# Kernel optimization log

Measured on AMD Instinct MI355X. Metric: run time of the kernel, lower is better.

## Reference

```python
import jax, jax.numpy as jnp
import numpy as np

N = 1024        # total atoms
H = 256         # hidden_dim
L = 512         # latent_dim
NG = 50         # n_gaussians
NI = 3          # n_interactions
CUTOFF = 5.0
MAXZ = 100
B = 16          # molecules (N // 64 atoms each)

CENTERS = jnp.linspace(0.0, CUTOFF, NG)
WIDTH = 0.5 * (CUTOFF / NG)   # scalar, same for all gaussians
LN_EPS = 1e-5

def gelu(x):
    return jax.nn.gelu(x, approximate=False)  # torch default GELU is exact erf

def setup_inputs() -> dict:
    key = jax.random.key(0)
    ks = jax.random.split(key, 24)
    s = 0.05
    inp = {
        'z': jax.random.randint(ks[0], (N,), 0, MAXZ),
        'pos': jax.random.uniform(ks[1], (N, 3), dtype=jnp.float32) * 10.0,  # 10 A box
        'batch': jnp.arange(N, dtype=jnp.int32) // (N // B),
        'emb': jax.random.normal(ks[2], (MAXZ, H), dtype=jnp.float32),
        # per-interaction params stacked over layer axis (NI)
        'fw1': jax.random.normal(ks[3], (NI, NG, H), dtype=jnp.float32) * s,
        'fb1': jnp.zeros((NI, H), jnp.float32),
        'fw2': jax.random.normal(ks[4], (NI, H, H), dtype=jnp.float32) * s,
        'fb2': jnp.zeros((NI, H), jnp.float32),
        'aw1': jax.random.normal(ks[5], (NI, H, H), dtype=jnp.float32) * s,
        'ab1': jnp.zeros((NI, H), jnp.float32),
        'aw2': jax.random.normal(ks[6], (NI, H, H), dtype=jnp.float32) * s,
        'ab2': jnp.zeros((NI, H), jnp.float32),
        # projection head
        'pw1': jax.random.normal(ks[7], (H, H), dtype=jnp.float32) * s,
        'pb1': jnp.zeros((H,), jnp.float32),
        'pw2': jax.random.normal(ks[8], (H, L), dtype=jnp.float32) * s,
        'pb2': jnp.zeros((L,), jnp.float32),
        'ln_g': jnp.ones((L,), jnp.float32),
        'ln_b': jnp.zeros((L,), jnp.float32),
    }
    return inp

def _interaction(h, pos, fw1, fb1, fw2, fb2, aw1, ab1, aw2, ab2):
    diff = pos[None, :, :] - pos[:, None, :]              # [N,N,3]
    dist = jnp.linalg.norm(diff, axis=-1)                  # [N,N]
    mask = (dist < CUTOFF) & (dist > 1e-6)                 # [N,N]
    rbf = jnp.exp(-((dist[..., None] - CENTERS) ** 2) / (2.0 * WIDTH ** 2))  # [N,N,NG]
    W = gelu(rbf @ fw1 + fb1) @ fw2 + fb2                  # [N,N,H] filter MLP
    Wm = W * mask[..., None].astype(W.dtype)
    # agg[i,c] = sum_j Wm[i,j,c] * h[j,c]
    agg = jnp.einsum('ijc,jc->ic', Wm, h)
    return gelu(agg @ aw1 + ab1) @ aw2 + ab2

def reference(z, pos, batch, emb, fw1, fb1, fw2, fb2, aw1, ab1, aw2, ab2,
              pw1, pb1, pw2, pb2, ln_g, ln_b):
    h = emb[z]                                             # [N,H]
    for i in range(NI):
        h = h + _interaction(h, pos, fw1[i], fb1[i], fw2[i], fb2[i],
                             aw1[i], ab1[i], aw2[i], ab2[i])
    pooled = jax.ops.segment_sum(h, batch, num_segments=B)  # [B,H]
    x = gelu(pooled @ pw1 + pb1) @ pw2 + pb2               # [B,L]
    mu = jnp.mean(x, axis=-1, keepdims=True)
    var = jnp.var(x, axis=-1, keepdims=True)
    return (x - mu) / jnp.sqrt(var + LN_EPS) * ln_g + ln_b
```

## Files before the change

### kernel.cpp

```cpp
#include <hip/hip_runtime.h>
#include <hip/hip_fp16.h>
#include <math.h>

#define N 1024
#define H 256
#define L 512
#define NG 50
#define NI 3
#define B 16
#define NBINS 2048
#define CUT 5.0f
#define BPB 16
#define TROWS (NBINS + 1)
#define MATB 4
#define CAP 768
#define APAD 264

typedef __attribute__((ext_vector_type(8))) short bf16x8;
typedef __attribute__((ext_vector_type(4))) float f32x4;

#define FMA4(A_, S_, V_) do { \
    (A_).x = fmaf((S_), (V_).x, (A_).x); (A_).y = fmaf((S_), (V_).y, (A_).y); \
    (A_).z = fmaf((S_), (V_).z, (A_).z); (A_).w = fmaf((S_), (V_).w, (A_).w); } while (0)

__device__ __forceinline__ float gelu_f(float x) {
    return 0.5f * x * (1.0f + erff(x * 0.70710678118654752f));
}
__device__ __forceinline__ unsigned short f2bf(float f) {
    unsigned u = __float_as_uint(f);
    unsigned r = (u + 0x7fffu + ((u >> 16) & 1u)) >> 16;
    return (unsigned short)r;
}

__global__ void __launch_bounds__(256) setup_k(
        const int* __restrict__ z, const float* __restrict__ emb,
        const float* __restrict__ pos, float* __restrict__ h,
        __half* __restrict__ hhf, int* __restrict__ meta,
        int* __restrict__ cnts, const float* __restrict__ fw2,
        unsigned short* __restrict__ Bt, __half* __restrict__ Wtb) {
    int tid = threadIdx.x;
    if (blockIdx.x >= N) {
        int blk = blockIdx.x - N;
        int l = blk / H, ch = blk % H;
        float v = fw2[((size_t)l * H + tid) * H + ch];
        Bt[((size_t)l * H + ch) * H + tid] = f2bf(v);
        if (tid == 0)
            Wtb[((size_t)l * TROWS + NBINS) * H + ch] = __float2half(0.f);
        return;
    }
    int i = blockIdx.x;
    float v = emb[z[i] * H + tid];
    h[i * H + tid] = v;
    hhf[i * H + tid] = __float2half(v);

    __shared__ int sCnt;
    __shared__ int sMeta[CAP];
    if (tid == 0) sCnt = 0;
    __syncthreads();
    float pix = pos[i * 3 + 0], piy = pos[i * 3 + 1], piz = pos[i * 3 + 2];
    const float invd = (float)NBINS / CUT;
    int lane = tid & 63;
    for (int r = 0; r < 4; ++r) {
        int j = tid + r * 256;
        float dx = pos[j * 3 + 0] - pix;
        float dy = pos[j * 3 + 1] - piy;
        float dz = pos[j * 3 + 2] - piz;
        float d = sqrtf(dx * dx + dy * dy + dz * dz);
        bool keep = (d < CUT && d > 1e-6f);
        unsigned long long mk = __ballot(keep);
        int base = 0;
        if (lane == 0) base = atomicAdd(&sCnt, (int)__popcll(mk));
        base = __shfl(base, 0);
        if (keep) {
            int bin = (int)(d * invd);
            if (bin > NBINS - 1) bin = NBINS - 1;
            int off = (int)__popcll(mk & ((1ull << lane) - 1ull));
            sMeta[base + off] = j | (bin << 10);
        }
    }
    __syncthreads();
    int cnt = sCnt;
    int pc = (cnt + 31) & ~31;
    for (int t = cnt + tid; t < pc; t += 256)
        sMeta[t] = i | (NBINS << 10);
    __syncthreads();
    for (int t = tid; t < pc; t += 256)
        meta[(size_t)i * CAP + t] = sMeta[t];
    if (tid == 0) cnts[i] = pc;
}

__global__ void __launch_bounds__(256) table_k(
        const float* __restrict__ fw1, const float* __restrict__ fb1,
        const unsigned short* __restrict__ Bt, const float* __restrict__ fb2,
        __half* __restrict__ Wtb) {
    const int bpl = NBINS / BPB;
    int layer = blockIdx.x / bpl;
    int blk = blockIdx.x % bpl;
    int b0 = blk * BPB;
    int tid = threadIdx.x;
    int wid = tid >> 6, lane = tid & 63;
    int c4 = lane * 4;
    int ub = wid * 4;
    const float* lfw1 = fw1 + layer * NG * H;
    __half* lWt = Wtb + (size_t)layer * TROWS * H;

    __shared__ __align__(16) float sW1[NG][H];
    __shared__ __align__(16) float sRbf[BPB][56];
    __shared__ __align__(16) unsigned short sAb[BPB][APAD];
    const float delta = CUT / (float)NBINS;
    for (int idx = tid; idx < NG * (H / 4); idx += 256) {
        int k = idx >> 6;
        int c = (idx & 63) * 4;
        *(float4*)&sW1[k][c] = *(const float4*)(lfw1 + k * H + c);
    }
    for (int idx = tid; idx < BPB * NG; idx += 256) {
        int u = idx & 15;
        int k = idx >> 4;
        float d = ((float)(b0 + u) + 0.5f) * delta;
        float t = d - (float)k * (CUT / 49.0f);
        sRbf[u][k] = expf(t * t * -200.0f);
    }
    __syncthreads();

    float4 acc1[4];
    #pragma unroll
    for (int u = 0; u < 4; ++u) acc1[u] = make_float4(0.f, 0.f, 0.f, 0.f);
    for (int kq = 0; kq < 12; ++kq) {
        int k = kq * 4;
        float4 r0 = *(const float4*)&sRbf[ub + 0][k];
        float4 r1 = *(const float4*)&sRbf[ub + 1][k];
        float4 r2 = *(const float4*)&sRbf[ub + 2][k];
        float4 r3 = *(const float4*)&sRbf[ub + 3][k];
        float4 q0 = *(const float4*)&sW1[k + 0][c4];
        float4 q1 = *(const float4*)&sW1[k + 1][c4];
        float4 q2 = *(const float4*)&sW1[k + 2][c4];
        float4 q3 = *(const float4*)&sW1[k + 3][c4];
        FMA4(acc1[0], r0.x, q0); FMA4(acc1[0], r0.y, q1);
        FMA4(acc1[0], r0.z, q2); FMA4(acc1[0], r0.w, q3);
        FMA4(acc1[1], r1.x, q0); FMA4(acc1[1], r1.y, q1);
        FMA4(acc1[1], r1.z, q2); FMA4(acc1[1], r1.w, q3);
        FMA4(acc1[2], r2.x, q0); FMA4(acc1[2], r2.y, q1);
        FMA4(acc1[2], r2.z, q2); FMA4(acc1[2], r2.w, q3);
        FMA4(acc1[3], r3.x, q0); FMA4(acc1[3], r3.y, q1);
        FMA4(acc1[3], r3.z, q2); FMA4(acc1[3], r3.w, q3);
    }
    for (int k = 48; k < NG; ++k) {
        float4 q = *(const float4*)&sW1[k][c4];
        #pragma unroll
        for (int u = 0; u < 4; ++u) FMA4(acc1[u], sRbf[ub + u][k], q);
    }
    float4 b1 = *(const float4*)(fb1 + layer * H + c4);
    #pragma unroll
    for (int u = 0; u < 4; ++u) {
        ushort4 g;
        g.x = f2bf(gelu_f(acc1[u].x + b1.x));
        g.y = f2bf(gelu_f(acc1[u].y + b1.y));
        g.z = f2bf(gelu_f(acc1[u].z + b1.z));
        g.w = f2bf(gelu_f(acc1[u].w + b1.w));
        *(ushort4*)&sAb[ub + u][c4] = g;
    }
    __syncthreads();

    int m = lane & 15;
    int quad = lane >> 4;
    bf16x8 afr[8];
    #pragma unroll
    for (int c = 0; c < 8; ++c)
        afr[c] = *(const bf16x8*)&sAb[m][c * 32 + quad * 8];
    #pragma unroll
    for (int ct = 0; ct < 4; ++ct) {
        int chn = (wid * 4 + ct) * 16 + m;
        const bf16x8* Bv = (const bf16x8*)(Bt + ((size_t)layer * H + chn) * H);
        f32x4 acc = {0.f, 0.f, 0.f, 0.f};
        #pragma unroll
        for (int c = 0; c < 8; ++c)
            acc = __builtin_amdgcn_mfma_f32_16x16x32_bf16(afr[c], Bv[c * 4 + quad],
                                                          acc, 0, 0, 0);
        float bias = fb2[layer * H + chn];
        #pragma unroll
        for (int r = 0; r < 4; ++r) {
            int bin = b0 + quad * 4 + r;
            lWt[(size_t)bin * H + chn] = __float2half(acc[r] + bias);
        }
    }
}

__global__ void __launch_bounds__(256) pair_k(
    const __half* __restrict__ hhf, const __half* __restrict__ Wt,
    const int* __restrict__ gmeta, const int* __restrict__ cnts,
    float* __restrict__ aggP) {
    int tid = threadIdx.x;
    int wid = tid >> 6, lane = tid & 63;
    int c4 = lane * 4;
    int i = blockIdx.x >> 1;
    int half = blockIdx.x & 1;
    int stream = half * 4 + wid;

    __shared__ __align__(16) float sPart[4][H];

    int pc = cnts[i];
    int len = pc >> 3;
    int chunks = len >> 2;
    int sbase = __builtin_amdgcn_readfirstlane(stream * len);
    const int* mptr = gmeta + (size_t)i * CAP + sbase;
    const char* WtB = (const char*)Wt;
    const char* hhB = (const char*)hhf;
    int choffB = lane * 8;

    float4 acc = make_float4(0.f, 0.f, 0.f, 0.f);
    int4 mA, mB;
    uint2 wA[4], hA[4], wB[4], hB[4];

    auto ldmeta = [&](int c) -> int4 {
        return *(const int4*)(mptr + c * 4);
    };
    auto one = [&](int p, uint2& wr, uint2& hr) {
        p = __builtin_amdgcn_readfirstlane(p);
        int j = p & 1023;
        int bin = p >> 10;
        wr = *(const uint2*)(WtB + (((unsigned)bin << 9) | (unsigned)choffB));
        hr = *(const uint2*)(hhB + (((unsigned)j << 9) | (unsigned)choffB));
    };
    auto issueD = [&](const int4& m, uint2 (&wr)[4], uint2 (&hr)[4]) {
        one(m.x, wr[0], hr[0]); one(m.y, wr[1], hr[1]);
        one(m.z, wr[2], hr[2]); one(m.w, wr[3], hr[3]);
    };
    auto consume = [&](uint2 (&wr)[4], uint2 (&hr)[4]) {
        #pragma unroll
        for (int u = 0; u < 4; ++u) {
            __half2 w01 = *(__half2*)&wr[u].x;
            __half2 w23 = *(__half2*)&wr[u].y;
            __half2 h01 = *(__half2*)&hr[u].x;
            __half2 h23 = *(__half2*)&hr[u].y;
            acc.x += __half2float(w01.x) * __half2float(h01.x);
            acc.y += __half2float(w01.y) * __half2float(h01.y);
            acc.z += __half2float(w23.x) * __half2float(h23.x);
            acc.w += __half2float(w23.y) * __half2float(h23.y);
        }
    };

    if (chunks > 0) {
        mA = ldmeta(0);
        if (chunks > 1) mB = ldmeta(1);
        issueD(mA, wA, hA);
        for (int c = 0; c < chunks; c += 2) {
            if (c + 2 < chunks) mA = ldmeta(c + 2);
            if (c + 1 < chunks) issueD(mB, wB, hB);
            consume(wA, hA);
            if (c + 3 < chunks) mB = ldmeta(c + 3);
            if (c + 2 < chunks) issueD(mA, wA, hA);
            if (c + 1 < chunks) consume(wB, hB);
        }
    }
    *(float4*)&sPart[wid][c4] = acc;
    __syncthreads();
    aggP[((size_t)half * N + i) * H + tid] =
        sPart[0][tid] + sPart[1][tid] + sPart[2][tid] + sPart[3][tid];
}

__global__ void __launch_bounds__(512) mlp_k(
    const float* __restrict__ aggP, const float* __restrict__ hin,
    const float* __restrict__ aw1, const float* __restrict__ ab1,
    const float* __restrict__ aw2, const float* __restrict__ ab2,
    float* __restrict__ hout, __half* __restrict__ hhf_out) {
    int tid = threadIdx.x;
    int wid = tid >> 6, lane = tid & 63;
    int c4 = lane * 4;
    int i0 = blockIdx.x * MATB;
    __shared__ __align__(16) float sAT[H][MATB];
    __shared__ __align__(16) float sGT[H][MATB];
    __shared__ __align__(16) float sPart[8][MATB][H];

    if (tid < H) {
        #pragma unroll
        for (int r = 0; r < MATB; ++r)
            sAT[tid][r] = aggP[(size_t)(i0 + r) * H + tid]
                        + aggP[((size_t)N + i0 + r) * H + tid];
    }
    __syncthreads();

    int k0 = wid * 32;
    float4 acc[MATB];
    #pragma unroll
    for (int a = 0; a < MATB; ++a) acc[a] = make_float4(0.f, 0.f, 0.f, 0.f);
    #pragma unroll 8
    for (int k = 0; k < 32; ++k) {
        float4 q = *(const float4*)(aw1 + (k0 + k) * H + c4);
        float4 act = *(const float4*)&sAT[k0 + k][0];
        FMA4(acc[0], act.x, q); FMA4(acc[1], act.y, q);
        FMA4(acc[2], act.z, q); FMA4(acc[3], act.w, q);
    }
    #pragma unroll
    for (int a = 0; a < MATB; ++a)
        *(float4*)&sPart[wid][a][c4] = acc[a];
    __syncthreads();
    if (tid < H) {
        float b1 = ab1[tid];
        float g[MATB];
        #pragma unroll
        for (int a = 0; a < MATB; ++a) {
            float v = b1;
            #pragma unroll
            for (int s = 0; s < 8; ++s) v += sPart[s][a][tid];
            g[a] = gelu_f(v);
        }
        *(float4*)&sGT[tid][0] = make_float4(g[0], g[1], g[2], g[3]);
    }
    __syncthreads();
    #pragma unroll
    for (int a = 0; a < MATB; ++a) acc[a] = make_float4(0.f, 0.f, 0.f, 0.f);
    #pragma unroll 8
    for (int k = 0; k < 32; ++k) {
        float4 q = *(const float4*)(aw2 + (k0 + k) * H + c4);
        float4 act = *(const float4*)&sGT[k0 + k][0];
        FMA4(acc[0], act.x, q); FMA4(acc[1], act.y, q);
        FMA4(acc[2], act.z, q); FMA4(acc[3], act.w, q);
    }
    #pragma unroll
    for (int a = 0; a < MATB; ++a)
        *(float4*)&sPart[wid][a][c4] = acc[a];
    __syncthreads();
    if (tid < H) {
        float b2 = ab2[tid];
        #pragma unroll
        for (int a = 0; a < MATB; ++a) {
            float v = b2;
            #pragma unroll
            for (int s = 0; s < 8; ++s) v += sPart[s][a][tid];
            float hv = hin[(i0 + a) * H + tid] + v;
            hout[(i0 + a) * H + tid] = hv;
            hhf_out[(i0 + a) * H + tid] = __float2half(hv);
        }
    }
}

__global__ void __launch_bounds__(256) head_k(
        const float* __restrict__ h,
        const float* __restrict__ pw1, const float* __restrict__ pb1,
        const float* __restrict__ pw2, const float* __restrict__ pb2,
        const float* __restrict__ ln_g, const float* __restrict__ ln_b,
        float* __restrict__ out) {
    int b = blockIdx.x, tid = threadIdx.x;
    int wid = tid >> 6, lane = tid & 63;
    int c4 = lane * 4;
    __shared__ float sP[H];
    __shared__ __align__(16) float sPw[4][H];
    __shared__ float sG[H];
    __shared__ __align__(16) float sP2[4][L];
    __shared__ float sX[L];
    __shared__ float sRed[256];

    float4 p = make_float4(0.f, 0.f, 0.f, 0.f);
    #pragma unroll 4
    for (int a = 0; a < 16; ++a) {
        float4 hv = *(const float4*)(h + (b * 64 + wid * 16 + a) * H + c4);
        p.x += hv.x; p.y += hv.y; p.z += hv.z; p.w += hv.w;
    }
    *(float4*)&sPw[wid][c4] = p;
    __syncthreads();
    sP[tid] = sPw[0][tid] + sPw[1][tid] + sPw[2][tid] + sPw[3][tid];
    __syncthreads();

    int k0 = wid * 64;
    float4 acc = make_float4(0.f, 0.f, 0.f, 0.f);
    #pragma unroll 8
    for (int k = 0; k < 64; ++k) {
        float4 q = *(const float4*)(pw1 + (k0 + k) * H + c4);
        float s = sP[k0 + k];
        FMA4(acc, s, q);
    }
    *(float4*)&sPw[wid][c4] = acc;
    __syncthreads();
    sG[tid] = gelu_f(pb1[tid] + sPw[0][tid] + sPw[1][tid] + sPw[2][tid] + sPw[3][tid]);
    __syncthreads();

    float4 a0 = make_float4(0.f, 0.f, 0.f, 0.f);
    float4 a1 = make_float4(0.f, 0.f, 0.f, 0.f);
    #pragma unroll 4
    for (int k = 0; k < 64; ++k) {
        float s = sG[k0 + k];
        float4 q0 = *(const float4*)(pw2 + (k0 + k) * L + lane * 8);
        float4 q1 = *(const float4*)(pw2 + (k0 + k) * L + lane * 8 + 4);
        FMA4(a0, s, q0);
        FMA4(a1, s, q1);
    }
    *(float4*)&sP2[wid][lane * 8] = a0;
    *(float4*)&sP2[wid][lane * 8 + 4] = a1;
    __syncthreads();
    for (int r = 0; r < 2; ++r) {
        int l = tid + r * 256;
        sX[l] = pb2[l] + sP2[0][l] + sP2[1][l] + sP2[2][l] + sP2[3][l];
    }
    __syncthreads();

    sRed[tid] = sX[tid] + sX[tid + 256];
    __syncthreads();
    for (int off = 128; off > 0; off >>= 1) {
        if (tid < off) sRed[tid] += sRed[tid + off];
        __syncthreads();
    }
    float mu = sRed[0] / (float)L;
    __syncthreads();
    float d0 = sX[tid] - mu, d1 = sX[tid + 256] - mu;
    sRed[tid] = d0 * d0 + d1 * d1;
    __syncthreads();
    for (int off = 128; off > 0; off >>= 1) {
        if (tid < off) sRed[tid] += sRed[tid + off];
        __syncthreads();
    }
    float var = sRed[0] / (float)L;
    float rstd = rsqrtf(var + 1e-5f);
    for (int r = 0; r < 2; ++r) {
        int l = tid + r * 256;
        out[b * L + l] = (sX[l] - mu) * rstd * ln_g[l] + ln_b[l];
    }
}

extern "C" void kernel_launch(void* const* d_in, const int* in_sizes, int n_in,
                              void* d_out, int out_size, void* d_ws, size_t ws_size,
                              hipStream_t stream) {
    const int*   z    = (const int*)d_in[0];
    const float* pos  = (const float*)d_in[1];
    const float* emb  = (const float*)d_in[3];
    const float* fw1  = (const float*)d_in[4];
    const float* fb1  = (const float*)d_in[5];
    const float* fw2  = (const float*)d_in[6];
    const float* fb2  = (const float*)d_in[7];
    const float* aw1  = (const float*)d_in[8];
    const float* ab1  = (const float*)d_in[9];
    const float* aw2  = (const float*)d_in[10];
    const float* ab2  = (const float*)d_in[11];
    const float* pw1  = (const float*)d_in[12];
    const float* pb1  = (const float*)d_in[13];
    const float* pw2  = (const float*)d_in[14];
    const float* pb2  = (const float*)d_in[15];
    const float* ln_g = (const float*)d_in[16];
    const float* ln_b = (const float*)d_in[17];
    float* out = (float*)d_out;

    float* hA  = (float*)d_ws;
    float* hB  = hA + N * H;
    float* aggP = hB + N * H;
    __half* hhfA = (__half*)(aggP + 2 * N * H);
    __half* hhfB = hhfA + N * H;
    __half* Wtb  = hhfB + N * H;
    int* meta = (int*)(Wtb + (size_t)NI * TROWS * H);
    int* cnts = meta + (size_t)N * CAP;
    unsigned short* Bt = (unsigned short*)(cnts + N);

    setup_k<<<N + NI * H, 256, 0, stream>>>(z, emb, pos, hA, hhfA, meta, cnts,
                                            fw2, Bt, Wtb);
    table_k<<<NI * (NBINS / BPB), 256, 0, stream>>>(fw1, fb1, Bt, fb2, Wtb);
    float* hin = hA;  __half* hbin = hhfA;
    float* hout = hB; __half* hbout = hhfB;
    for (int it = 0; it < NI; ++it) {
        pair_k<<<2 * N, 256, 0, stream>>>(hbin, Wtb + (size_t)it * TROWS * H,
                                          meta, cnts, aggP);
        mlp_k<<<N / MATB, 512, 0, stream>>>(aggP, hin, aw1 + it * H * H, ab1 + it * H,
                                            aw2 + it * H * H, ab2 + it * H, hout, hbout);
        float* t1 = hin; hin = hout; hout = t1;
        __half* t2 = hbin; hbin = hbout; hbout = t2;
    }
    head_k<<<B, 256, 0, stream>>>(hin, pw1, pb1, pw2, pb2, ln_g, ln_b, out);
}
```

Measured before the change: 233.1 us.

## Fuse all stages into one persistent cooperative kernel with grid syncs

Replaces the sequence of eight kernel launches (setup, table, three pair/mlp pairs, head) with a single persistent cooperative kernel that loops over work items and uses grid.sync between stages. The aim is to remove launch overhead and inter-kernel gaps. In exchange, grid size is capped at occupancy times 256 blocks, so per-stage parallelism changes. The pair stage now runs one block per atom instead of 2N blocks, and the mlp stage uses 256 threads instead of 512. The original multi-kernel path is kept as a fallback if the cooperative launch fails.

```diff
diff --git a/kernel.cpp b/kernel.cpp
--- a/kernel.cpp
+++ b/kernel.cpp
@@ -1,6 +1,9 @@
 #include <hip/hip_runtime.h>
 #include <hip/hip_fp16.h>
+#include <hip/hip_cooperative_groups.h>
 #include <math.h>
+
+namespace cg = cooperative_groups;
 
 #define N 1024
 #define H 256
@@ -15,6 +18,7 @@
 #define MATB 4
 #define CAP 768
 #define APAD 264
+#define KH 24
 
 typedef __attribute__((ext_vector_type(8))) short bf16x8;
 typedef __attribute__((ext_vector_type(4))) float f32x4;
@@ -221,9 +225,9 @@
         wr = *(const uint2*)(WtB + (((unsigned)bin << 9) | (unsigned)choffB));
         hr = *(const uint2*)(hhB + (((unsigned)j << 9) | (unsigned)choffB));
     };
-    auto issueD = [&](const int4& m, uint2 (&wr)[4], uint2 (&hr)[4]) {
-        one(m.x, wr[0], hr[0]); one(m.y, wr[1], hr[1]);
-        one(m.z, wr[2], hr[2]); one(m.w, wr[3], hr[3]);
+    auto issueD = [&](const int4& m4, uint2 (&wr)[4], uint2 (&hr)[4]) {
+        one(m4.x, wr[0], hr[0]); one(m4.y, wr[1], hr[1]);
+        one(m4.z, wr[2], hr[2]); one(m4.w, wr[3], hr[3]);
     };
     auto consume = [&](uint2 (&wr)[4], uint2 (&hr)[4]) {
         #pragma unroll
@@ -413,6 +417,393 @@
     for (int r = 0; r < 2; ++r) {
         int l = tid + r * 256;
         out[b * L + l] = (sX[l] - mu) * rstd * ln_g[l] + ln_b[l];
+    }
+}
+
+struct SetupS { int cnt; int meta[CAP]; };
+struct TableS { float w1[KH][H]; float rbf[BPB][56]; unsigned short ab[BPB][APAD]; };
+struct PairS  { float part[4][H]; };
+struct MlpS   { float at[H][MATB]; float gt[H][MATB]; float part[4][MATB][H]; };
+struct HeadS  { float p[H]; float pw[4][H]; float g[H]; float p2[4][L]; float x[L]; float red[256]; };
+union __align__(16) SharedU { SetupS su; TableS tb; PairS pr; MlpS ml; HeadS hd; };
+
+__global__ void __launch_bounds__(256, 2) mega_k(
+        const int* __restrict__ z, const float* __restrict__ pos,
+        const float* __restrict__ emb,
+        const float* __restrict__ fw1, const float* __restrict__ fb1,
+        const float* __restrict__ fw2, const float* __restrict__ fb2,
+        const float* __restrict__ aw1, const float* __restrict__ ab1,
+        const float* __restrict__ aw2, const float* __restrict__ ab2,
+        const float* __restrict__ pw1, const float* __restrict__ pb1,
+        const float* __restrict__ pw2, const float* __restrict__ pb2,
+        const float* __restrict__ ln_g, const float* __restrict__ ln_b,
+        float* __restrict__ out,
+        float* __restrict__ hbuf0, float* __restrict__ hbuf1,
+        float* __restrict__ agg,
+        __half* __restrict__ hhalf0, __half* __restrict__ hhalf1,
+        __half* __restrict__ Wtb, int* __restrict__ meta,
+        int* __restrict__ cnts, unsigned short* __restrict__ Bt) {
+    cg::grid_group grid = cg::this_grid();
+    __shared__ SharedU S;
+    int tid = threadIdx.x;
+    int wid = tid >> 6, lane = tid & 63;
+    int c4 = lane * 4;
+
+    for (int item = blockIdx.x; item < N + NI * H; item += gridDim.x) {
+        if (item >= N) {
+            int blk = item - N;
+            int l = blk / H, ch = blk % H;
+            float v = fw2[((size_t)l * H + tid) * H + ch];
+            Bt[((size_t)l * H + ch) * H + tid] = f2bf(v);
+            if (tid == 0)
+                Wtb[((size_t)l * TROWS + NBINS) * H + ch] = __float2half(0.f);
+            continue;
+        }
+        int i = item;
+        float v = emb[z[i] * H + tid];
+        hbuf0[i * H + tid] = v;
+        hhalf0[i * H + tid] = __float2half(v);
+
+        if (tid == 0) S.su.cnt = 0;
+        __syncthreads();
+        float pix = pos[i * 3 + 0], piy = pos[i * 3 + 1], piz = pos[i * 3 + 2];
+        const float invd = (float)NBINS / CUT;
+        for (int r = 0; r < 4; ++r) {
+            int j = tid + r * 256;
+            float dx = pos[j * 3 + 0] - pix;
+            float dy = pos[j * 3 + 1] - piy;
+            float dz = pos[j * 3 + 2] - piz;
+            float d = sqrtf(dx * dx + dy * dy + dz * dz);
+            bool keep = (d < CUT && d > 1e-6f);
+            unsigned long long mk = __ballot(keep);
+            int base = 0;
+            if (lane == 0) base = atomicAdd(&S.su.cnt, (int)__popcll(mk));
+            base = __shfl(base, 0);
+            if (keep) {
+                int bin = (int)(d * invd);
+                if (bin > NBINS - 1) bin = NBINS - 1;
+                int off = (int)__popcll(mk & ((1ull << lane) - 1ull));
+                S.su.meta[base + off] = j | (bin << 10);
+            }
+        }
+        __syncthreads();
+        int cnt = S.su.cnt;
+        int pc = (cnt + 31) & ~31;
+        for (int t = cnt + tid; t < pc; t += 256)
+            S.su.meta[t] = i | (NBINS << 10);
+        __syncthreads();
+        for (int t = tid; t < pc; t += 256)
+            meta[(size_t)i * CAP + t] = S.su.meta[t];
+        if (tid == 0) cnts[i] = pc;
+        __syncthreads();
+    }
+    __threadfence();
+    grid.sync();
+
+    for (int item = blockIdx.x; item < NI * (NBINS / BPB); item += gridDim.x) {
+        int layer = item / (NBINS / BPB);
+        int blk = item % (NBINS / BPB);
+        int b0 = blk * BPB;
+        int ub = wid * 4;
+        const float* lfw1 = fw1 + layer * NG * H;
+        __half* lWt = Wtb + (size_t)layer * TROWS * H;
+        const float delta = CUT / (float)NBINS;
+
+        for (int idx = tid; idx < BPB * NG; idx += 256) {
+            int u = idx & 15, k = idx >> 4;
+            float d = ((float)(b0 + u) + 0.5f) * delta;
+            float t = d - (float)k * (CUT / 49.0f);
+            S.tb.rbf[u][k] = expf(t * t * -200.0f);
+        }
+        float4 q48 = *(const float4*)(lfw1 + 48 * H + c4);
+        float4 q49 = *(const float4*)(lfw1 + 49 * H + c4);
+
+        float4 acc1[4];
+        #pragma unroll
+        for (int u = 0; u < 4; ++u) acc1[u] = make_float4(0.f, 0.f, 0.f, 0.f);
+        #pragma unroll
+        for (int hf = 0; hf < 2; ++hf) {
+            int kb = hf * KH;
+            if (hf) __syncthreads();
+            for (int idx = tid; idx < KH * (H / 4); idx += 256) {
+                int k = idx >> 6, c = (idx & 63) * 4;
+                *(float4*)&S.tb.w1[k][c] = *(const float4*)(lfw1 + (kb + k) * H + c);
+            }
+            __syncthreads();
+            for (int kq = 0; kq < KH / 4; ++kq) {
+                int k = kq * 4;
+                float4 r0 = *(const float4*)&S.tb.rbf[ub + 0][kb + k];
+                float4 r1 = *(const float4*)&S.tb.rbf[ub + 1][kb + k];
+                float4 r2 = *(const float4*)&S.tb.rbf[ub + 2][kb + k];
+                float4 r3 = *(const float4*)&S.tb.rbf[ub + 3][kb + k];
+                float4 q0 = *(const float4*)&S.tb.w1[k + 0][c4];
+                float4 q1 = *(const float4*)&S.tb.w1[k + 1][c4];
+                float4 q2 = *(const float4*)&S.tb.w1[k + 2][c4];
+                float4 q3 = *(const float4*)&S.tb.w1[k + 3][c4];
+                FMA4(acc1[0], r0.x, q0); FMA4(acc1[0], r0.y, q1);
+                FMA4(acc1[0], r0.z, q2); FMA4(acc1[0], r0.w, q3);
+                FMA4(acc1[1], r1.x, q0); FMA4(acc1[1], r1.y, q1);
+                FMA4(acc1[1], r1.z, q2); FMA4(acc1[1], r1.w, q3);
+                FMA4(acc1[2], r2.x, q0); FMA4(acc1[2], r2.y, q1);
+                FMA4(acc1[2], r2.z, q2); FMA4(acc1[2], r2.w, q3);
+                FMA4(acc1[3], r3.x, q0); FMA4(acc1[3], r3.y, q1);
+                FMA4(acc1[3], r3.z, q2); FMA4(acc1[3], r3.w, q3);
+            }
+        }
+        #pragma unroll
+        for (int u = 0; u < 4; ++u) {
+            FMA4(acc1[u], S.tb.rbf[ub + u][48], q48);
+            FMA4(acc1[u], S.tb.rbf[ub + u][49], q49);
+        }
+        float4 b1 = *(const float4*)(fb1 + layer * H + c4);
+        #pragma unroll
+        for (int u = 0; u < 4; ++u) {
+            ushort4 g;
+            g.x = f2bf(gelu_f(acc1[u].x + b1.x));
+            g.y = f2bf(gelu_f(acc1[u].y + b1.y));
+            g.z = f2bf(gelu_f(acc1[u].z + b1.z));
+            g.w = f2bf(gelu_f(acc1[u].w + b1.w));
+            *(ushort4*)&S.tb.ab[ub + u][c4] = g;
+        }
+        __syncthreads();
+
+        int m = lane & 15;
+        int quad = lane >> 4;
+        bf16x8 afr[8];
+        #pragma unroll
+        for (int c = 0; c < 8; ++c)
+            afr[c] = *(const bf16x8*)&S.tb.ab[m][c * 32 + quad * 8];
+        #pragma unroll
+        for (int ct = 0; ct < 4; ++ct) {
+            int chn = (wid * 4 + ct) * 16 + m;
+            const bf16x8* Bv = (const bf16x8*)(Bt + ((size_t)layer * H + chn) * H);
+            f32x4 acc = {0.f, 0.f, 0.f, 0.f};
+            #pragma unroll
+            for (int c = 0; c < 8; ++c)
+                acc = __builtin_amdgcn_mfma_f32_16x16x32_bf16(afr[c], Bv[c * 4 + quad],
+                                                              acc, 0, 0, 0);
+            float bias = fb2[layer * H + chn];
+            #pragma unroll
+            for (int r = 0; r < 4; ++r) {
+                int bin = b0 + quad * 4 + r;
+                lWt[(size_t)bin * H + chn] = __float2half(acc[r] + bias);
+            }
+        }
+        __syncthreads();
+    }
+    __threadfence();
+    grid.sync();
+
+    const float* hi = hbuf0;  float* ho = hbuf1;
+    const __half* hfi = hhalf0; __half* hfo = hhalf1;
+    for (int itn = 0; itn < NI; ++itn) {
+        const __half* Wt = Wtb + (size_t)itn * TROWS * H;
+        const float* aw1i = aw1 + itn * H * H;
+        const float* ab1i = ab1 + itn * H;
+        const float* aw2i = aw2 + itn * H * H;
+        const float* ab2i = ab2 + itn * H;
+
+        for (int i = blockIdx.x; i < N; i += gridDim.x) {
+            int pc = cnts[i];
+            int len = pc >> 2;
+            int chunks = len >> 2;
+            int sbase = __builtin_amdgcn_readfirstlane(wid * len);
+            const int* mptr = meta + (size_t)i * CAP + sbase;
+            const char* WtB = (const char*)Wt;
+            const char* hhB = (const char*)hfi;
+            int choffB = lane * 8;
+
+            float4 acc = make_float4(0.f, 0.f, 0.f, 0.f);
+            int4 mA, mB;
+            uint2 wA[4], hA[4], wB[4], hB[4];
+
+            auto ldmeta = [&](int c) -> int4 {
+                return *(const int4*)(mptr + c * 4);
+            };
+            auto one = [&](int p, uint2& wr, uint2& hr) {
+                p = __builtin_amdgcn_readfirstlane(p);
+                int j = p & 1023;
+                int bin = p >> 10;
+                wr = *(const uint2*)(WtB + (((unsigned)bin << 9) | (unsigned)choffB));
+                hr = *(const uint2*)(hhB + (((unsigned)j << 9) | (unsigned)choffB));
+            };
+            auto issueD = [&](const int4& m4, uint2 (&wr)[4], uint2 (&hr)[4]) {
+                one(m4.x, wr[0], hr[0]); one(m4.y, wr[1], hr[1]);
+                one(m4.z, wr[2], hr[2]); one(m4.w, wr[3], hr[3]);
+            };
+            auto consume = [&](uint2 (&wr)[4], uint2 (&hr)[4]) {
+                #pragma unroll
+                for (int u = 0; u < 4; ++u) {
+                    __half2 w01 = *(__half2*)&wr[u].x;
+                    __half2 w23 = *(__half2*)&wr[u].y;
+                    __half2 h01 = *(__half2*)&hr[u].x;
+                    __half2 h23 = *(__half2*)&hr[u].y;
+                    acc.x += __half2float(w01.x) * __half2float(h01.x);
+                    acc.y += __half2float(w01.y) * __half2float(h01.y);
+                    acc.z += __half2float(w23.x) * __half2float(h23.x);
+                    acc.w += __half2float(w23.y) * __half2float(h23.y);
+                }
+            };
+
+            if (chunks > 0) {
+                mA = ldmeta(0);
+                if (chunks > 1) mB = ldmeta(1);
+                issueD(mA, wA, hA);
+                for (int c = 0; c < chunks; c += 2) {
+                    if (c + 2 < chunks) mA = ldmeta(c + 2);
+                    if (c + 1 < chunks) issueD(mB, wB, hB);
+                    consume(wA, hA);
+                    if (c + 3 < chunks) mB = ldmeta(c + 3);
+                    if (c + 2 < chunks) issueD(mA, wA, hA);
+                    if (c + 1 < chunks) consume(wB, hB);
+                }
+            }
+            *(float4*)&S.pr.part[wid][c4] = acc;
+            __syncthreads();
+            agg[(size_t)i * H + tid] = S.pr.part[0][tid] + S.pr.part[1][tid]
+                                     + S.pr.part[2][tid] + S.pr.part[3][tid];
+            __syncthreads();
+        }
+        __threadfence();
+        grid.sync();
+
+        for (int it2 = blockIdx.x; it2 < N / MATB; it2 += gridDim.x) {
+            int i0 = it2 * MATB;
+            #pragma unroll
+            for (int r = 0; r < MATB; ++r)
+                S.ml.at[tid][r] = agg[(size_t)(i0 + r) * H + tid];
+            __syncthreads();
+
+            int k0 = wid * 64;
+            float4 acc[MATB];
+            #pragma unroll
+            for (int a = 0; a < MATB; ++a) acc[a] = make_float4(0.f, 0.f, 0.f, 0.f);
+            #pragma unroll 8
+            for (int k = 0; k < 64; ++k) {
+                float4 q = *(const float4*)(aw1i + (k0 + k) * H + c4);
+                float4 act = *(const float4*)&S.ml.at[k0 + k][0];
+                FMA4(acc[0], act.x, q); FMA4(acc[1], act.y, q);
+                FMA4(acc[2], act.z, q); FMA4(acc[3], act.w, q);
+            }
+            #pragma unroll
+            for (int a = 0; a < MATB; ++a)
+                *(float4*)&S.ml.part[wid][a][c4] = acc[a];
+            __syncthreads();
+            {
+                float b1v = ab1i[tid];
+                float g[MATB];
+                #pragma unroll
+                for (int a = 0; a < MATB; ++a) {
+                    float v = b1v;
+                    #pragma unroll
+                    for (int s = 0; s < 4; ++s) v += S.ml.part[s][a][tid];
+                    g[a] = gelu_f(v);
+                }
+                *(float4*)&S.ml.gt[tid][0] = make_float4(g[0], g[1], g[2], g[3]);
+            }
+            __syncthreads();
+            #pragma unroll
+            for (int a = 0; a < MATB; ++a) acc[a] = make_float4(0.f, 0.f, 0.f, 0.f);
+            #pragma unroll 8
+            for (int k = 0; k < 64; ++k) {
+                float4 q = *(const float4*)(aw2i + (k0 + k) * H + c4);
+                float4 act = *(const float4*)&S.ml.gt[k0 + k][0];
+                FMA4(acc[0], act.x, q); FMA4(acc[1], act.y, q);
+                FMA4(acc[2], act.z, q); FMA4(acc[3], act.w, q);
+            }
+            #pragma unroll
+            for (int a = 0; a < MATB; ++a)
+                *(float4*)&S.ml.part[wid][a][c4] = acc[a];
+            __syncthreads();
+            {
+                float b2v = ab2i[tid];
+                #pragma unroll
+                for (int a = 0; a < MATB; ++a) {
+                    float v = b2v;
+                    #pragma unroll
+                    for (int s = 0; s < 4; ++s) v += S.ml.part[s][a][tid];
+                    float hv = hi[(size_t)(i0 + a) * H + tid] + v;
+                    ho[(size_t)(i0 + a) * H + tid] = hv;
+                    hfo[(size_t)(i0 + a) * H + tid] = __float2half(hv);
+                }
+            }
+            __syncthreads();
+        }
+        __threadfence();
+        grid.sync();
+
+        const float* t1 = hi; hi = ho; ho = (float*)t1;
+        const __half* t2 = hfi; hfi = hfo; hfo = (__half*)t2;
+    }
+
+    for (int b = blockIdx.x; b < B; b += gridDim.x) {
+        float4 p = make_float4(0.f, 0.f, 0.f, 0.f);
+        #pragma unroll 4
+        for (int a = 0; a < 16; ++a) {
+            float4 hv = *(const float4*)(hi + (size_t)(b * 64 + wid * 16 + a) * H + c4);
+            p.x += hv.x; p.y += hv.y; p.z += hv.z; p.w += hv.w;
+        }
+        *(float4*)&S.hd.pw[wid][c4] = p;
+        __syncthreads();
+        S.hd.p[tid] = S.hd.pw[0][tid] + S.hd.pw[1][tid] + S.hd.pw[2][tid] + S.hd.pw[3][tid];
+        __syncthreads();
+
+        int k0 = wid * 64;
+        float4 acc = make_float4(0.f, 0.f, 0.f, 0.f);
+        #pragma unroll 8
+        for (int k = 0; k < 64; ++k) {
+            float4 q = *(const float4*)(pw1 + (k0 + k) * H + c4);
+            float s = S.hd.p[k0 + k];
+            FMA4(acc, s, q);
+        }
+        *(float4*)&S.hd.pw[wid][c4] = acc;
+        __syncthreads();
+        S.hd.g[tid] = gelu_f(pb1[tid] + S.hd.pw[0][tid] + S.hd.pw[1][tid]
+                             + S.hd.pw[2][tid] + S.hd.pw[3][tid]);
+        __syncthreads();
+
+        float4 a0 = make_float4(0.f, 0.f, 0.f, 0.f);
+        float4 a1 = make_float4(0.f, 0.f, 0.f, 0.f);
+        #pragma unroll 4
+        for (int k = 0; k < 64; ++k) {
+            float s = S.hd.g[k0 + k];
+            float4 q0 = *(const float4*)(pw2 + (k0 + k) * L + lane * 8);
+            float4 q1 = *(const float4*)(pw2 + (k0 + k) * L + lane * 8 + 4);
+            FMA4(a0, s, q0);
+            FMA4(a1, s, q1);
+        }
+        *(float4*)&S.hd.p2[wid][lane * 8] = a0;
+        *(float4*)&S.hd.p2[wid][lane * 8 + 4] = a1;
+        __syncthreads();
+        for (int r = 0; r < 2; ++r) {
+            int l = tid + r * 256;
+            S.hd.x[l] = pb2[l] + S.hd.p2[0][l] + S.hd.p2[1][l]
+                      + S.hd.p2[2][l] + S.hd.p2[3][l];
+        }
+        __syncthreads();
+
+        S.hd.red[tid] = S.hd.x[tid] + S.hd.x[tid + 256];
+        __syncthreads();
+        for (int off = 128; off > 0; off >>= 1) {
+            if (tid < off) S.hd.red[tid] += S.hd.red[tid + off];
+            __syncthreads();
+        }
+        float mu = S.hd.red[0] / (float)L;
+        __syncthreads();
+        float d0 = S.hd.x[tid] - mu, d1 = S.hd.x[tid + 256] - mu;
+        S.hd.red[tid] = d0 * d0 + d1 * d1;
+        __syncthreads();
+        for (int off = 128; off > 0; off >>= 1) {
+            if (tid < off) S.hd.red[tid] += S.hd.red[tid + off];
+            __syncthreads();
+        }
+        float var = S.hd.red[0] / (float)L;
+        float rstd = rsqrtf(var + 1e-5f);
+        for (int r = 0; r < 2; ++r) {
+            int l = tid + r * 256;
+            out[b * L + l] = (S.hd.x[l] - mu) * rstd * ln_g[l] + ln_b[l];
+        }
+        __syncthreads();
     }
 }
 
@@ -438,28 +829,50 @@
     const float* ln_b = (const float*)d_in[17];
     float* out = (float*)d_out;
 
-    float* hA  = (float*)d_ws;
-    float* hB  = hA + N * H;
-    float* aggP = hB + N * H;
-    __half* hhfA = (__half*)(aggP + 2 * N * H);
-    __half* hhfB = hhfA + N * H;
-    __half* Wtb  = hhfB + N * H;
+    float* hbuf0 = (float*)d_ws;
+    float* hbuf1 = hbuf0 + N * H;
+    float* agg   = hbuf1 + N * H;
+    __half* hhalf0 = (__half*)(agg + 2 * N * H);
+    __half* hhalf1 = hhalf0 + N * H;
+    __half* Wtb  = hhalf1 + N * H;
     int* meta = (int*)(Wtb + (size_t)NI * TROWS * H);
     int* cnts = meta + (size_t)N * CAP;
     unsigned short* Bt = (unsigned short*)(cnts + N);
 
-    setup_k<<<N + NI * H, 256, 0, stream>>>(z, emb, pos, hA, hhfA, meta, cnts,
-                                            fw2, Bt, Wtb);
-    table_k<<<NI * (NBINS / BPB), 256, 0, stream>>>(fw1, fb1, Bt, fb2, Wtb);
-    float* hin = hA;  __half* hbin = hhfA;
-    float* hout = hB; __half* hbout = hhfB;
-    for (int it = 0; it < NI; ++it) {
-        pair_k<<<2 * N, 256, 0, stream>>>(hbin, Wtb + (size_t)it * TROWS * H,
-                                          meta, cnts, aggP);
-        mlp_k<<<N / MATB, 512, 0, stream>>>(aggP, hin, aw1 + it * H * H, ab1 + it * H,
-                                            aw2 + it * H * H, ab2 + it * H, hout, hbout);
-        float* t1 = hin; hin = hout; hout = t1;
-        __half* t2 = hbin; hbin = hbout; hbout = t2;
-    }
-    head_k<<<B, 256, 0, stream>>>(hin, pw1, pb1, pw2, pb2, ln_g, ln_b, out);
+    static int occ = -1;
+    if (occ < 0) {
+        int q = 0;
+        if (hipOccupancyMaxActiveBlocksPerMultiprocessor(&q, mega_k, 256, 0)
+                != hipSuccess || q < 1)
+            q = 2;
+        if (q > 4) q = 4;
+        occ = q;
+    }
+    int nblk = occ * 256;
+    if (nblk > 1024) nblk = 1024;
+
+    void* args[] = { &z, &pos, &emb, &fw1, &fb1, &fw2, &fb2, &aw1, &ab1,
+                     &aw2, &ab2, &pw1, &pb1, &pw2, &pb2, &ln_g, &ln_b, &out,
+                     &hbuf0, &hbuf1, &agg, &hhalf0, &hhalf1, &Wtb, &meta,
+                     &cnts, &Bt };
+    hipError_t e = hipLaunchCooperativeKernel(mega_k, dim3(nblk), dim3(256),
+                                              args, 0, stream);
+    if (e != hipSuccess) {
+        (void)hipGetLastError();
+        setup_k<<<N + NI * H, 256, 0, stream>>>(z, emb, pos, hbuf0, hhalf0,
+                                                meta, cnts, fw2, Bt, Wtb);
+        table_k<<<NI * (NBINS / BPB), 256, 0, stream>>>(fw1, fb1, Bt, fb2, Wtb);
+        float* hin = hbuf0;  __half* hbin = hhalf0;
+        float* hout = hbuf1; __half* hbout = hhalf1;
+        for (int it = 0; it < NI; ++it) {
+            pair_k<<<2 * N, 256, 0, stream>>>(hbin, Wtb + (size_t)it * TROWS * H,
+                                              meta, cnts, agg);
+            mlp_k<<<N / MATB, 512, 0, stream>>>(agg, hin, aw1 + it * H * H,
+                                                ab1 + it * H, aw2 + it * H * H,
+                                                ab2 + it * H, hout, hbout);
+            float* t1 = hin; hin = hout; hout = t1;
+            __half* t2 = hbin; hbin = hbout; hbout = t2;
+        }
+        head_k<<<B, 256, 0, stream>>>(hin, pw1, pb1, pw2, pb2, ln_g, ln_b, out);
+    }
 }
```

New measurement: 704.4 us. 3.02x slower.

## Split pair neighbor lists into fixed segments with atomic accumulation

Applied to the files above, without the earlier changes.

Each atom's neighbor list is now split into fixed 256-entry segments, with up to three blocks per atom. Blocks past the end of the list exit immediately, so launched work follows the actual neighbor count instead of a fixed half split. Partial sums are combined with float atomicAdd into a single aggregate buffer, which mlp_k reads and then zeroes for the next layer. This brings atomic contention and non-deterministic summation order, and padded per-segment lengths (rem>>2, then >>2) may drop tail neighbors differently than before.

```diff
diff --git a/kernel.cpp b/kernel.cpp
--- a/kernel.cpp
+++ b/kernel.cpp
@@ -14,6 +14,7 @@
 #define TROWS (NBINS + 1)
 #define MATB 4
 #define CAP 768
+#define SEGSZ 256
 #define APAD 264
 
 typedef __attribute__((ext_vector_type(8))) short bf16x8;
@@ -37,7 +38,8 @@
         const float* __restrict__ pos, float* __restrict__ h,
         __half* __restrict__ hhf, int* __restrict__ meta,
         int* __restrict__ cnts, const float* __restrict__ fw2,
-        unsigned short* __restrict__ Bt, __half* __restrict__ Wtb) {
+        unsigned short* __restrict__ Bt, __half* __restrict__ Wtb,
+        float* __restrict__ agg) {
     int tid = threadIdx.x;
     if (blockIdx.x >= N) {
         int blk = blockIdx.x - N;
@@ -52,6 +54,7 @@
     float v = emb[z[i] * H + tid];
     h[i * H + tid] = v;
     hhf[i * H + tid] = __float2half(v);
+    agg[(size_t)i * H + tid] = 0.f;
 
     __shared__ int sCnt;
     __shared__ int sMeta[CAP];
@@ -188,20 +191,23 @@
 __global__ void __launch_bounds__(256) pair_k(
     const __half* __restrict__ hhf, const __half* __restrict__ Wt,
     const int* __restrict__ gmeta, const int* __restrict__ cnts,
-    float* __restrict__ aggP) {
+    float* __restrict__ agg) {
     int tid = threadIdx.x;
     int wid = tid >> 6, lane = tid & 63;
     int c4 = lane * 4;
-    int i = blockIdx.x >> 1;
-    int half = blockIdx.x & 1;
-    int stream = half * 4 + wid;
+    int b = blockIdx.x;
+    int i = b / 3;
+    int seg = b - i * 3;
+    int pc = cnts[i];
+    int sb = seg * SEGSZ;
+    if (sb >= pc) return;
+    int rem = pc - sb; if (rem > SEGSZ) rem = SEGSZ;
+    int len = rem >> 2;
+    int chunks = len >> 2;
 
     __shared__ __align__(16) float sPart[4][H];
 
-    int pc = cnts[i];
-    int len = pc >> 3;
-    int chunks = len >> 2;
-    int sbase = __builtin_amdgcn_readfirstlane(stream * len);
+    int sbase = __builtin_amdgcn_readfirstlane(sb + wid * len);
     const int* mptr = gmeta + (size_t)i * CAP + sbase;
     const char* WtB = (const char*)Wt;
     const char* hhB = (const char*)hhf;
@@ -221,9 +227,9 @@
         wr = *(const uint2*)(WtB + (((unsigned)bin << 9) | (unsigned)choffB));
         hr = *(const uint2*)(hhB + (((unsigned)j << 9) | (unsigned)choffB));
     };
-    auto issueD = [&](const int4& m, uint2 (&wr)[4], uint2 (&hr)[4]) {
-        one(m.x, wr[0], hr[0]); one(m.y, wr[1], hr[1]);
-        one(m.z, wr[2], hr[2]); one(m.w, wr[3], hr[3]);
+    auto issueD = [&](const int4& m4, uint2 (&wr)[4], uint2 (&hr)[4]) {
+        one(m4.x, wr[0], hr[0]); one(m4.y, wr[1], hr[1]);
+        one(m4.z, wr[2], hr[2]); one(m4.w, wr[3], hr[3]);
     };
     auto consume = [&](uint2 (&wr)[4], uint2 (&hr)[4]) {
         #pragma unroll
@@ -254,12 +260,12 @@
     }
     *(float4*)&sPart[wid][c4] = acc;
     __syncthreads();
-    aggP[((size_t)half * N + i) * H + tid] =
-        sPart[0][tid] + sPart[1][tid] + sPart[2][tid] + sPart[3][tid];
+    float v = sPart[0][tid] + sPart[1][tid] + sPart[2][tid] + sPart[3][tid];
+    atomicAdd(&agg[(size_t)i * H + tid], v);
 }
 
 __global__ void __launch_bounds__(512) mlp_k(
-    const float* __restrict__ aggP, const float* __restrict__ hin,
+    float* __restrict__ agg, const float* __restrict__ hin,
     const float* __restrict__ aw1, const float* __restrict__ ab1,
     const float* __restrict__ aw2, const float* __restrict__ ab2,
     float* __restrict__ hout, __half* __restrict__ hhf_out) {
@@ -273,9 +279,10 @@
 
     if (tid < H) {
         #pragma unroll
-        for (int r = 0; r < MATB; ++r)
-            sAT[tid][r] = aggP[(size_t)(i0 + r) * H + tid]
-                        + aggP[((size_t)N + i0 + r) * H + tid];
+        for (int r = 0; r < MATB; ++r) {
+            sAT[tid][r] = agg[(size_t)(i0 + r) * H + tid];
+            agg[(size_t)(i0 + r) * H + tid] = 0.f;
+        }
     }
     __syncthreads();
 
@@ -440,8 +447,8 @@
 
     float* hA  = (float*)d_ws;
     float* hB  = hA + N * H;
-    float* aggP = hB + N * H;
-    __half* hhfA = (__half*)(aggP + 2 * N * H);
+    float* agg = hB + N * H;
+    __half* hhfA = (__half*)(agg + 2 * N * H);
     __half* hhfB = hhfA + N * H;
     __half* Wtb  = hhfB + N * H;
     int* meta = (int*)(Wtb + (size_t)NI * TROWS * H);
@@ -449,14 +456,14 @@
     unsigned short* Bt = (unsigned short*)(cnts + N);
 
     setup_k<<<N + NI * H, 256, 0, stream>>>(z, emb, pos, hA, hhfA, meta, cnts,
-                                            fw2, Bt, Wtb);
+                                            fw2, Bt, Wtb, agg);
     table_k<<<NI * (NBINS / BPB), 256, 0, stream>>>(fw1, fb1, Bt, fb2, Wtb);
     float* hin = hA;  __half* hbin = hhfA;
     float* hout = hB; __half* hbout = hhfB;
     for (int it = 0; it < NI; ++it) {
-        pair_k<<<2 * N, 256, 0, stream>>>(hbin, Wtb + (size_t)it * TROWS * H,
-                                          meta, cnts, aggP);
-        mlp_k<<<N / MATB, 512, 0, stream>>>(aggP, hin, aw1 + it * H * H, ab1 + it * H,
+        pair_k<<<3 * N, 256, 0, stream>>>(hbin, Wtb + (size_t)it * TROWS * H,
+                                          meta, cnts, agg);
+        mlp_k<<<N / MATB, 512, 0, stream>>>(agg, hin, aw1 + it * H * H, ab1 + it * H,
                                             aw2 + it * H * H, ab2 + it * H, hout, hbout);
         float* t1 = hin; hin = hout; hout = t1;
         __half* t2 = hbin; hbin = hbout; hbout = t2;
```

Measured after the change: 243.3 us. 1.04x slower.
